# Kernel tuning notes

Hardware: AMD Instinct MI355X
Metric: run time of the kernel (lower is better)

Reference implementation:

```python
import jax, jax.numpy as jnp
import numpy as np

N = 50000          # num nodes
E = 800000         # edges per adjacency
NUM_A = 4          # number of adjacency matrices
C = 2              # num_channels
D_IN = 128
D_OUT = 64


def setup_inputs() -> dict:
    key = jax.random.key(0)
    k1, k2, k3, k4, k5, k6 = jax.random.split(key, 6)
    H = jax.random.normal(k1, (N, D_IN), dtype=jnp.float32)
    vals = jax.random.uniform(k2, (NUM_A, E), dtype=jnp.float32)
    rows = jax.random.randint(k3, (NUM_A, E), 0, N, dtype=jnp.int32)
    cols = jax.random.randint(k4, (NUM_A, E), 0, N, dtype=jnp.int32)
    # xavier-ish init for learned params
    weight = jax.random.normal(k5, (C, D_IN, D_OUT), dtype=jnp.float32) * (2.0 / (D_IN + D_OUT)) ** 0.5
    att_weight = jax.random.normal(k6, (C, D_IN, NUM_A), dtype=jnp.float32) * (2.0 / (D_IN + NUM_A)) ** 0.5
    return {"H": H, "vals": vals, "weight": weight, "att_weight": att_weight,
            "rows": rows, "cols": cols}


def reference(H, vals, weight, att_weight, rows, cols):
    # H: [N, in], weight: [C, in, out], att_weight: [C, in, num_A]
    # rows/cols/vals: [num_A, E] COO edge lists for each sparse adjacency A_i
    n = H.shape[0]
    num_channels = weight.shape[0]
    Hc_all = jnp.einsum('nd,cdo->cno', H, weight)            # [C, N, out]
    score = jax.nn.softmax(att_weight.mean(axis=1), axis=1)   # [C, num_A]
    r = rows.reshape(-1)                                      # [num_A*E]
    cl = cols.reshape(-1)
    outs = []
    for c in range(num_channels):
        # A_combined = sum_i score[c, i] * A_i, applied as SpMM via segment_sum
        w = (score[c][:, None] * vals).reshape(-1)            # [num_A*E]
        msgs = Hc_all[c][cl] * w[:, None]                     # [num_A*E, out]
        outs.append(jax.ops.segment_sum(msgs, r, num_segments=n))
    return jnp.mean(jnp.stack(outs, axis=0), axis=0)          # [N, out]
```

## Files before the change

### kernel.cpp

```cpp
#include <hip/hip_runtime.h>

constexpr int D_IN  = 128;
constexpr int D_OUT = 64;
constexpr int NCH   = 2;
constexpr int NUM_A = 4;
constexpr int COLS  = NCH * D_OUT;
constexpr int RPB   = 64;
constexpr int MAXNB = 800;
constexpr int CAP   = 4608;
constexpr int SPT   = 512;
constexpr int RPT   = CAP / SPT;
constexpr int CAPB  = 6144;

typedef __attribute__((ext_vector_type(8))) short bf16x8;
typedef __attribute__((ext_vector_type(4))) float f32x4;

__device__ inline unsigned short f2bf_rn(float f) {
    unsigned u = __float_as_uint(f);
    return (unsigned short)((u + 0x7fffu + ((u >> 16) & 1u)) >> 16);
}

__global__ __launch_bounds__(64) void score_kernel(const float* __restrict__ att,
                                                   float* __restrict__ score,
                                                   unsigned* __restrict__ cinit,
                                                   int NB, int padded) {
    int lane = threadIdx.x;
    for (int i = lane; i < NB; i += 64)
        cinit[i] = padded ? (unsigned)i * (unsigned)CAPB : 0u;
    int c = lane >> 2, a = lane & 3;
    float s = 0.0f;
    if (lane < 8) {
        const float* p = att + c * (D_IN * NUM_A) + a;
        for (int d = 0; d < D_IN; ++d) s += p[d * NUM_A];
        s *= (1.0f / D_IN);
    }
    float m = fmaxf(s, __shfl_xor(s, 1));
    m = fmaxf(m, __shfl_xor(m, 2));
    float ex = __expf(s - m);
    float sum = ex + __shfl_xor(ex, 1);
    sum += __shfl_xor(sum, 2);
    if (lane < 8) score[lane] = 0.5f * ex / sum;
}

__global__ __launch_bounds__(256) void gemm_kernel(const float* __restrict__ H,
                                                   const float* __restrict__ W,
                                                   unsigned short* __restrict__ Hc, int N) {
    __shared__ unsigned short Bs[128 * 136];

    const int t = threadIdx.x;
    for (int i = t; i < 128 * 128; i += 256) {
        const int k = i >> 7, n = i & 127;
        const int c = n >> 6, nn = n & 63;
        Bs[n * 136 + k] = f2bf_rn(W[c * (D_IN * D_OUT) + k * D_OUT + nn]);
    }

    const int lane = t & 63;
    const int wr   = t >> 6;
    const int kg   = lane >> 4;
    const int l15  = lane & 15;
    const int row0 = blockIdx.x * 64;

    int arow = row0 + wr * 16 + l15;
    if (arow >= N) arow = N - 1;

    bf16x8 afrag[4];
    const float* hrow = H + (size_t)arow * D_IN;
    #pragma unroll
    for (int s = 0; s < 4; ++s) {
        const int k0 = s * 32 + kg * 8;
        const float4 f0 = *reinterpret_cast<const float4*>(hrow + k0);
        const float4 f1 = *reinterpret_cast<const float4*>(hrow + k0 + 4);
        bf16x8 av;
        av[0] = (short)f2bf_rn(f0.x); av[1] = (short)f2bf_rn(f0.y);
        av[2] = (short)f2bf_rn(f0.z); av[3] = (short)f2bf_rn(f0.w);
        av[4] = (short)f2bf_rn(f1.x); av[5] = (short)f2bf_rn(f1.y);
        av[6] = (short)f2bf_rn(f1.z); av[7] = (short)f2bf_rn(f1.w);
        afrag[s] = av;
    }
    __syncthreads();

    #pragma unroll
    for (int nt = 0; nt < 8; ++nt) {
        const int n = nt * 16 + l15;
        f32x4 acc = {0.f, 0.f, 0.f, 0.f};
        #pragma unroll
        for (int s = 0; s < 4; ++s) {
            const bf16x8 bfrag =
                *reinterpret_cast<const bf16x8*>(&Bs[n * 136 + s * 32 + kg * 8]);
            acc = __builtin_amdgcn_mfma_f32_16x16x32_bf16(afrag[s], bfrag, acc, 0, 0, 0);
        }
        #pragma unroll
        for (int r = 0; r < 4; ++r) {
            const int drow = row0 + wr * 16 + kg * 4 + r;
            if (drow < N) Hc[(size_t)drow * COLS + n] = f2bf_rn(acc[r]);
        }
    }
}

__global__ __launch_bounds__(1024) void hist_kernel(const int* __restrict__ rows,
                                                    unsigned* __restrict__ counts,
                                                    int TE, int NB) {
    __shared__ unsigned h[MAXNB];
    const int t = threadIdx.x;
    for (int i = t; i < MAXNB; i += 1024) h[i] = 0u;
    __syncthreads();
    for (int e = blockIdx.x * 1024 + t; e < TE; e += gridDim.x * 1024)
        atomicAdd(&h[rows[e] >> 6], 1u);
    __syncthreads();
    for (int i = t; i < NB; i += 1024)
        if (h[i]) atomicAdd(&counts[i], h[i]);
}

__global__ __launch_bounds__(1024) void scan_kernel(const unsigned* __restrict__ counts,
                                                    unsigned* __restrict__ offsets,
                                                    unsigned* __restrict__ cursor, int n) {
    __shared__ unsigned part[1024];
    const int t = threadIdx.x;
    const int chunk = (n + 1023) >> 10;
    const int s = t * chunk;
    const int e = min(s + chunk, n);
    unsigned sum = 0;
    for (int i = s; i < e; ++i) sum += counts[i];
    part[t] = sum;
    __syncthreads();
    for (int d = 1; d < 1024; d <<= 1) {
        unsigned v = (t >= d) ? part[t - d] : 0u;
        __syncthreads();
        part[t] += v;
        __syncthreads();
    }
    unsigned run = (t == 0) ? 0u : part[t - 1];
    for (int i = s; i < e; ++i) {
        const unsigned c = counts[i];
        offsets[i] = run;
        cursor[i]  = run;
        run += c;
    }
}

constexpr int SC_T   = 1024;
constexpr int SC_EPT = 4;
constexpr int SC_CH  = SC_T * SC_EPT;

__global__ __launch_bounds__(SC_T) void scatter_kernel(const int* __restrict__ rows,
                                                       const int* __restrict__ cols,
                                                       const float* __restrict__ vals,
                                                       const float* __restrict__ score,
                                                       unsigned* __restrict__ cursor,
                                                       uint2* __restrict__ erec,
                                                       int TE, int Eper, int NB) {
    __shared__ unsigned lh[MAXNB];
    __shared__ unsigned lbase[MAXNB];
    __shared__ unsigned gbase[MAXNB];
    __shared__ unsigned part[SC_T];
    __shared__ __align__(16) uint2 srec[SC_CH];
    __shared__ unsigned sdst[SC_CH];
    __shared__ float ssc[8];

    const int t  = threadIdx.x;
    const int e0 = blockIdx.x * SC_CH;

    if (t < 8) ssc[t] = score[t];
    for (int i = t; i < MAXNB; i += SC_T) lh[i] = 0u;
    __syncthreads();

    unsigned bk[SC_EPT], rank[SC_EPT], meta[SC_EPT], wpk[SC_EPT];
    #pragma unroll
    for (int k = 0; k < SC_EPT; ++k) {
        const int e = e0 + k * SC_T + t;
        bk[k] = 0xffffffffu;
        if (e < TE) {
            const int row = rows[e];
            const int col = cols[e];
            const float v = vals[e];
            const int  a  = e / Eper;
            bk[k]   = (unsigned)(row >> 6);
            rank[k] = atomicAdd(&lh[bk[k]], 1u);
            meta[k] = (unsigned)col | ((unsigned)(row & 63) << 16);
            wpk[k]  = (unsigned)f2bf_rn(ssc[a] * v) |
                      ((unsigned)f2bf_rn(ssc[4 + a] * v) << 16);
        }
    }
    __syncthreads();

    const unsigned myc = (t < NB) ? lh[t] : 0u;
    part[t] = myc;
    __syncthreads();
    for (int d = 1; d < SC_T; d <<= 1) {
        unsigned v = (t >= d) ? part[t - d] : 0u;
        __syncthreads();
        part[t] += v;
        __syncthreads();
    }
    if (t < NB) {
        lbase[t] = part[t] - myc;
        gbase[t] = myc ? atomicAdd(&cursor[t], myc) : 0u;
    }
    __syncthreads();

    #pragma unroll
    for (int k = 0; k < SC_EPT; ++k) {
        if (bk[k] != 0xffffffffu) {
            const unsigned p = lbase[bk[k]] + rank[k];
            srec[p] = make_uint2(meta[k], wpk[k]);
            sdst[p] = gbase[bk[k]] + rank[k];
        }
    }
    __syncthreads();

    const unsigned cn = min((unsigned)(TE - e0), (unsigned)SC_CH);
    #pragma unroll
    for (int k = 0; k < SC_EPT; ++k) {
        const unsigned p = (unsigned)(k * SC_T + t);
        if (p < cn) erec[sdst[p]] = srec[p];
    }
}

__global__ __launch_bounds__(SPT) void bucketspmm_kernel(const uint2* __restrict__ erec,
                                                         const unsigned* __restrict__ offsets,
                                                         const unsigned* __restrict__ counts,
                                                         const unsigned* __restrict__ cursor,
                                                         const unsigned* __restrict__ Hc32,
                                                         float* __restrict__ out,
                                                         int N, int padded) {
    __shared__ __align__(16) uint2 srec[CAP];
    __shared__ unsigned roff8[8 * 68];
    __shared__ unsigned roff[RPB + 1];

    const int t    = threadIdx.x;
    const int lane = t & 63;
    const int w    = t >> 6;
    const int bucket = blockIdx.x;
    unsigned start, cnt;
    if (padded) {
        start = (unsigned)bucket * (unsigned)CAPB;
        cnt   = cursor[bucket] - start;
    } else {
        start = offsets[bucket];
        cnt   = counts[bucket];
    }
    const int wsh = (lane < 32) ? 16 : 0;

    float2 acc[8];
    #pragma unroll
    for (int r = 0; r < 8; ++r) acc[r] = make_float2(0.f, 0.f);

    for (unsigned cb = 0; cb < cnt; cb += CAP) {
        const unsigned cn = min(cnt - cb, (unsigned)CAP);

        for (int i = t; i < 8 * 68; i += SPT) roff8[i] = 0u;
        __syncthreads();

        uint2 rec[RPT];
        unsigned rank[RPT];
        #pragma unroll
        for (int k = 0; k < RPT; ++k) {
            const unsigned idx = (unsigned)(k * SPT + t);
            rec[k] = make_uint2(0xffffffffu, 0u);
            if (idx < cn) {
                rec[k] = erec[start + cb + idx];
                rank[k] = atomicAdd(&roff8[w * 68 + (rec[k].x >> 16)], 1u);
            }
        }
        __syncthreads();

        if (t < 64) {
            unsigned run = 0;
            #pragma unroll
            for (int w2 = 0; w2 < 8; ++w2) {
                const unsigned v = roff8[w2 * 68 + t];
                roff8[w2 * 68 + t] = run;
                run += v;
            }
            unsigned incl = run;
            #pragma unroll
            for (int d = 1; d < 64; d <<= 1) {
                const unsigned nb = __shfl_up(incl, d);
                if (lane >= d) incl += nb;
            }
            roff[t] = incl - run;
            if (t == 63) roff[RPB] = incl;
        }
        __syncthreads();

        #pragma unroll
        for (int k = 0; k < RPT; ++k) {
            if (rec[k].x != 0xffffffffu) {
                const unsigned rib = rec[k].x >> 16;
                const unsigned pos = roff[rib] + roff8[w * 68 + rib] + rank[k];
                srec[pos] = make_uint2(rec[k].x & 0xffffu, rec[k].y);
            }
        }
        __syncthreads();

        #pragma unroll
        for (int rr = 0; rr < 8; ++rr) {
            const int r = w * 8 + rr;
            unsigned j = roff[r];
            const unsigned e = roff[r + 1];
            float2 a = acc[rr];

            while (j + 16 <= e) {
                float    wv16[16];
                unsigned hv16[16];
                #pragma unroll
                for (int k = 0; k < 16; ++k) {
                    const uint2 rc = srec[j + k];
                    hv16[k] = Hc32[(rc.x << 6) + lane];
                    wv16[k] = __uint_as_float((rc.y << wsh) & 0xffff0000u);
                }
                #pragma unroll
                for (int k = 0; k < 16; ++k) {
                    a.x += wv16[k] * __uint_as_float(hv16[k] << 16);
                    a.y += wv16[k] * __uint_as_float(hv16[k] & 0xffff0000u);
                }
                j += 16;
            }
            while (j + 4 <= e) {
                float    wv4[4];
                unsigned hv4[4];
                #pragma unroll
                for (int k = 0; k < 4; ++k) {
                    const uint2 rc = srec[j + k];
                    hv4[k] = Hc32[(rc.x << 6) + lane];
                    wv4[k] = __uint_as_float((rc.y << wsh) & 0xffff0000u);
                }
                #pragma unroll
                for (int k = 0; k < 4; ++k) {
                    a.x += wv4[k] * __uint_as_float(hv4[k] << 16);
                    a.y += wv4[k] * __uint_as_float(hv4[k] & 0xffff0000u);
                }
                j += 4;
            }
            for (; j < e; ++j) {
                const uint2 rc = srec[j];
                const unsigned hv = Hc32[(rc.x << 6) + lane];
                const float wv = __uint_as_float((rc.y << wsh) & 0xffff0000u);
                a.x += wv * __uint_as_float(hv << 16);
                a.y += wv * __uint_as_float(hv & 0xffff0000u);
            }
            acc[rr] = a;
        }
        __syncthreads();
    }

    const int row0 = bucket * RPB + w * 8;
    #pragma unroll
    for (int rr = 0; rr < 8; ++rr) {
        float2 a = acc[rr];
        a.x += __shfl_xor(a.x, 32);
        a.y += __shfl_xor(a.y, 32);
        const int row = row0 + rr;
        if (lane < 32 && row < N) {
            *reinterpret_cast<float2*>(out + (size_t)row * D_OUT + lane * 2) = a;
        }
    }
}

extern "C" void kernel_launch(void* const* d_in, const int* in_sizes, int n_in,
                              void* d_out, int out_size, void* d_ws, size_t ws_size,
                              hipStream_t stream) {
    const float* H    = (const float*)d_in[0];
    const float* vals = (const float*)d_in[1];
    const float* W    = (const float*)d_in[2];
    const float* att  = (const float*)d_in[3];
    const int*   rows = (const int*)d_in[4];
    const int*   cols = (const int*)d_in[5];

    const int N    = in_sizes[0] / D_IN;
    const int TE   = in_sizes[1];
    const int Eper = TE / NUM_A;
    const int NB   = (N + RPB - 1) / RPB;

    char* ws = (char*)d_ws;
    size_t off = 0;
    float* ws_score = (float*)(ws + off);          off += 256;
    unsigned short* ws_Hc = (unsigned short*)(ws + off);
    off += (size_t)N * COLS * sizeof(unsigned short);
    off = (off + 255) & ~(size_t)255;
    unsigned* counts  = (unsigned*)(ws + off);     off += (size_t)MAXNB * sizeof(unsigned);
    unsigned* offsets = (unsigned*)(ws + off);     off += (size_t)MAXNB * sizeof(unsigned);
    unsigned* cursor  = (unsigned*)(ws + off);     off += (size_t)MAXNB * sizeof(unsigned);
    off = (off + 255) & ~(size_t)255;
    uint2* erec       = (uint2*)(ws + off);

    const size_t need_padded = off + (size_t)NB * CAPB * sizeof(uint2);
    const int padded = (ws_size >= need_padded) ? 1 : 0;

    score_kernel<<<1, 64, 0, stream>>>(att, ws_score, padded ? cursor : counts,
                                       NB, padded);

    gemm_kernel<<<(N + 63) / 64, 256, 0, stream>>>(H, W, ws_Hc, N);

    if (!padded) {
        hist_kernel<<<512, 1024, 0, stream>>>(rows, counts, TE, NB);
        scan_kernel<<<1, 1024, 0, stream>>>(counts, offsets, cursor, NB);
    }

    const int sblocks = (TE + SC_CH - 1) / SC_CH;
    scatter_kernel<<<sblocks, SC_T, 0, stream>>>(rows, cols, vals, ws_score,
                                                 cursor, erec, TE, Eper, NB);

    bucketspmm_kernel<<<NB, SPT, 0, stream>>>(erec, offsets, counts, cursor,
                                              (const unsigned*)ws_Hc,
                                              (float*)d_out, N, padded);
}
```

Before: 242.2 us.

## Switch Hc/weights to fp16 with packed hfma2, streamline scatter scan and records

```diff
diff --git a/kernel.cpp b/kernel.cpp
--- a/kernel.cpp
+++ b/kernel.cpp
@@ -1,4 +1,5 @@
 #include <hip/hip_runtime.h>
+#include <hip/hip_fp16.h>
 
 constexpr int D_IN  = 128;
 constexpr int D_OUT = 64;
@@ -18,6 +19,13 @@
 __device__ inline unsigned short f2bf_rn(float f) {
     unsigned u = __float_as_uint(f);
     return (unsigned short)((u + 0x7fffu + ((u >> 16) & 1u)) >> 16);
+}
+__device__ inline unsigned short f2h(float f) {
+    _Float16 h = (_Float16)f;
+    unsigned short u; __builtin_memcpy(&u, &h, 2); return u;
+}
+__device__ inline __half2 u2h2(unsigned u) {
+    __half2 h; __builtin_memcpy(&h, &u, 4); return h;
 }
 
 __global__ __launch_bounds__(64) void score_kernel(const float* __restrict__ att,
@@ -92,7 +100,7 @@
         #pragma unroll
         for (int r = 0; r < 4; ++r) {
             const int drow = row0 + wr * 16 + kg * 4 + r;
-            if (drow < N) Hc[(size_t)drow * COLS + n] = f2bf_rn(acc[r]);
+            if (drow < N) Hc[(size_t)drow * COLS + n] = f2h(acc[r]);
         }
     }
 }
@@ -139,7 +147,7 @@
 }
 
 constexpr int SC_T   = 1024;
-constexpr int SC_EPT = 4;
+constexpr int SC_EPT = 6;
 constexpr int SC_CH  = SC_T * SC_EPT;
 
 __global__ __launch_bounds__(SC_T) void scatter_kernel(const int* __restrict__ rows,
@@ -152,9 +160,8 @@
     __shared__ unsigned lh[MAXNB];
     __shared__ unsigned lbase[MAXNB];
     __shared__ unsigned gbase[MAXNB];
-    __shared__ unsigned part[SC_T];
+    __shared__ unsigned wsum[16];
     __shared__ __align__(16) uint2 srec[SC_CH];
-    __shared__ unsigned sdst[SC_CH];
     __shared__ float ssc[8];
 
     const int t  = threadIdx.x;
@@ -164,46 +171,57 @@
     for (int i = t; i < MAXNB; i += SC_T) lh[i] = 0u;
     __syncthreads();
 
-    unsigned bk[SC_EPT], rank[SC_EPT], meta[SC_EPT], wpk[SC_EPT];
+    unsigned bkrank[SC_EPT], meta[SC_EPT], wpk[SC_EPT];
     #pragma unroll
     for (int k = 0; k < SC_EPT; ++k) {
         const int e = e0 + k * SC_T + t;
-        bk[k] = 0xffffffffu;
+        bkrank[k] = 0xffffffffu;
         if (e < TE) {
             const int row = rows[e];
             const int col = cols[e];
             const float v = vals[e];
             const int  a  = e / Eper;
-            bk[k]   = (unsigned)(row >> 6);
-            rank[k] = atomicAdd(&lh[bk[k]], 1u);
-            meta[k] = (unsigned)col | ((unsigned)(row & 63) << 16);
-            wpk[k]  = (unsigned)f2bf_rn(ssc[a] * v) |
-                      ((unsigned)f2bf_rn(ssc[4 + a] * v) << 16);
-        }
-    }
-    __syncthreads();
-
-    const unsigned myc = (t < NB) ? lh[t] : 0u;
-    part[t] = myc;
-    __syncthreads();
-    for (int d = 1; d < SC_T; d <<= 1) {
-        unsigned v = (t >= d) ? part[t - d] : 0u;
-        __syncthreads();
-        part[t] += v;
-        __syncthreads();
-    }
+            const unsigned bk = (unsigned)(row >> 6);
+            const unsigned rk = atomicAdd(&lh[bk], 1u);
+            bkrank[k] = (bk << 16) | rk;
+            meta[k]   = (unsigned)col | ((unsigned)(row & 63) << 16) | (bk << 22);
+            wpk[k]    = (unsigned)f2h(ssc[a] * v) |
+                        ((unsigned)f2h(ssc[4 + a] * v) << 16);
+        }
+    }
+    __syncthreads();
+
+    const unsigned v = (t < NB) ? lh[t] : 0u;
+    unsigned incl = v;
+    #pragma unroll
+    for (int d = 1; d < 64; d <<= 1) {
+        const unsigned nb = __shfl_up(incl, d);
+        if ((t & 63) >= d) incl += nb;
+    }
+    if ((t & 63) == 63) wsum[t >> 6] = incl;
+    __syncthreads();
+    if (t < 16) {
+        const unsigned s = wsum[t];
+        unsigned i2 = s;
+        #pragma unroll
+        for (int d = 1; d < 16; d <<= 1) {
+            const unsigned nb = __shfl_up(i2, d);
+            if (t >= d) i2 += nb;
+        }
+        wsum[t] = i2 - s;
+    }
+    __syncthreads();
     if (t < NB) {
-        lbase[t] = part[t] - myc;
-        gbase[t] = myc ? atomicAdd(&cursor[t], myc) : 0u;
+        lbase[t] = incl - v + wsum[t >> 6];
+        gbase[t] = v ? atomicAdd(&cursor[t], v) : 0u;
     }
     __syncthreads();
 
     #pragma unroll
     for (int k = 0; k < SC_EPT; ++k) {
-        if (bk[k] != 0xffffffffu) {
-            const unsigned p = lbase[bk[k]] + rank[k];
+        if (bkrank[k] != 0xffffffffu) {
+            const unsigned p = lbase[bkrank[k] >> 16] + (bkrank[k] & 0xffffu);
             srec[p] = make_uint2(meta[k], wpk[k]);
-            sdst[p] = gbase[bk[k]] + rank[k];
         }
     }
     __syncthreads();
@@ -212,7 +230,12 @@
     #pragma unroll
     for (int k = 0; k < SC_EPT; ++k) {
         const unsigned p = (unsigned)(k * SC_T + t);
-        if (p < cn) erec[sdst[p]] = srec[p];
+        if (p < cn) {
+            const uint2 r = srec[p];
+            const unsigned bk = r.x >> 22;
+            const unsigned dst = gbase[bk] + (p - lbase[bk]);
+            erec[dst] = make_uint2(r.x & 0x003fffffu, r.y);
+        }
     }
 }
 
@@ -239,7 +262,7 @@
         start = offsets[bucket];
         cnt   = counts[bucket];
     }
-    const int wsh = (lane < 32) ? 16 : 0;
+    const unsigned psel = (lane < 32) ? 0x01000100u : 0x03020302u;
 
     float2 acc[8];
     #pragma unroll
@@ -301,43 +324,47 @@
             float2 a = acc[rr];
 
             while (j + 16 <= e) {
-                float    wv16[16];
-                unsigned hv16[16];
+                unsigned hv16[16], wv16[16];
                 #pragma unroll
                 for (int k = 0; k < 16; ++k) {
                     const uint2 rc = srec[j + k];
                     hv16[k] = Hc32[(rc.x << 6) + lane];
-                    wv16[k] = __uint_as_float((rc.y << wsh) & 0xffff0000u);
+                    wv16[k] = __builtin_amdgcn_perm(rc.y, rc.y, psel);
                 }
+                __half2 h2a = u2h2(0u), h2b = u2h2(0u);
                 #pragma unroll
-                for (int k = 0; k < 16; ++k) {
-                    a.x += wv16[k] * __uint_as_float(hv16[k] << 16);
-                    a.y += wv16[k] * __uint_as_float(hv16[k] & 0xffff0000u);
+                for (int k = 0; k < 16; k += 2) {
+                    h2a = __hfma2(u2h2(hv16[k]),     u2h2(wv16[k]),     h2a);
+                    h2b = __hfma2(u2h2(hv16[k + 1]), u2h2(wv16[k + 1]), h2b);
                 }
+                const __half2 hs = __hadd2(h2a, h2b);
+                a.x += __low2float(hs);
+                a.y += __high2float(hs);
                 j += 16;
             }
-            while (j + 4 <= e) {
-                float    wv4[4];
-                unsigned hv4[4];
-                #pragma unroll
-                for (int k = 0; k < 4; ++k) {
-                    const uint2 rc = srec[j + k];
-                    hv4[k] = Hc32[(rc.x << 6) + lane];
-                    wv4[k] = __uint_as_float((rc.y << wsh) & 0xffff0000u);
+            if (j < e) {
+                __half2 h2 = u2h2(0u);
+                while (j + 4 <= e) {
+                    unsigned hv4[4], wv4[4];
+                    #pragma unroll
+                    for (int k = 0; k < 4; ++k) {
+                        const uint2 rc = srec[j + k];
+                        hv4[k] = Hc32[(rc.x << 6) + lane];
+                        wv4[k] = __builtin_amdgcn_perm(rc.y, rc.y, psel);
+                    }
+                    #pragma unroll
+                    for (int k = 0; k < 4; ++k)
+                        h2 = __hfma2(u2h2(hv4[k]), u2h2(wv4[k]), h2);
+                    j += 4;
                 }
-                #pragma unroll
-                for (int k = 0; k < 4; ++k) {
-                    a.x += wv4[k] * __uint_as_float(hv4[k] << 16);
-                    a.y += wv4[k] * __uint_as_float(hv4[k] & 0xffff0000u);
+                for (; j < e; ++j) {
+                    const uint2 rc = srec[j];
+                    const unsigned hv = Hc32[(rc.x << 6) + lane];
+                    const unsigned wv = __builtin_amdgcn_perm(rc.y, rc.y, psel);
+                    h2 = __hfma2(u2h2(hv), u2h2(wv), h2);
                 }
-                j += 4;
-            }
-            for (; j < e; ++j) {
-                const uint2 rc = srec[j];
-                const unsigned hv = Hc32[(rc.x << 6) + lane];
-                const float wv = __uint_as_float((rc.y << wsh) & 0xffff0000u);
-                a.x += wv * __uint_as_float(hv << 16);
-                a.y += wv * __uint_as_float(hv & 0xffff0000u);
+                a.x += __low2float(h2);
+                a.y += __high2float(h2);
             }
             acc[rr] = a;
         }
```

New measurement: 233.4 us. -3.6%, faster.
